# Optimization experiments

Measured on AMD Instinct MI355X. Metric: run time of the kernel, lower is better.

Reference implementation:

```python
import jax, jax.numpy as jnp
import numpy as np

# Module config (matches init_kwargs)
DIM = 256
NUM_HEADS = 8
AREA = 4
B, C, H, W = 8, DIM, 64, 64
HEAD_DIM = DIM // NUM_HEADS

# Each Conv in the source is Conv2d(bias=False) + BatchNorm2d + Identity (activation=False).
# In eval mode BN is a per-channel affine, so we represent each Conv as (weight, scale, bias).

def setup_inputs() -> dict:
    key = jax.random.key(0)
    ks = jax.random.split(key, 13)
    def w(k, shape, s=0.05):
        return jax.random.normal(k, shape, jnp.float32) * s
    def bn_scale(k, n):
        return 1.0 + 0.02 * jax.random.normal(k, (n,), jnp.float32)
    x = jax.random.normal(ks[0], (B, C, H, W), jnp.float32)
    return {
        "x": x,
        "w_qk": w(ks[1], (2 * C, C)),        # 1x1 conv: [out,in]
        "s_qk": bn_scale(ks[2], 2 * C),
        "b_qk": w(ks[3], (2 * C,), 0.01),
        "w_v": w(ks[4], (C, C)),
        "s_v": bn_scale(ks[5], C),
        "b_v": w(ks[6], (C,), 0.01),
        "w_pe": w(ks[7], (C, 1, 5, 5)),       # depthwise 5x5, groups=C
        "s_pe": bn_scale(ks[8], C),
        "b_pe": w(ks[9], (C,), 0.01),
        "w_proj": w(ks[10], (C, C)),
        "s_proj": bn_scale(ks[11], C),
        "b_proj": w(ks[12], (C,), 0.01),
    }


def _affine(y, s, b):
    # per-channel BN-eval affine on NCHW
    return y * s[None, :, None, None] + b[None, :, None, None]


def _conv1x1(x, w, s, b):
    return _affine(jnp.einsum('bchw,oc->bohw', x, w), s, b)


def reference(x, w_qk, s_qk, b_qk, w_v, s_v, b_v, w_pe, s_pe, b_pe, w_proj, s_proj, b_proj):
    N = H * W
    Na = N // AREA
    Ba = B * AREA

    qk = _conv1x1(x, w_qk, s_qk, b_qk)                    # [B, 2C, H, W]
    v4 = _conv1x1(x, w_v, s_v, b_v)                       # [B, C, H, W]
    pp = _affine(
        jax.lax.conv_general_dilated(
            v4, w_pe, (1, 1), 'SAME', feature_group_count=C,
            dimension_numbers=('NCHW', 'OIHW', 'NCHW')),
        s_pe, b_pe)                                        # [B, C, H, W]

    # flatten(2).transpose(1,2) then area split along N
    qk = qk.reshape(B, 2 * C, N).transpose(0, 2, 1).reshape(Ba, Na, 2 * C)
    v = v4.reshape(B, C, N).transpose(0, 2, 1).reshape(Ba, Na, C)

    q = qk[..., :C].reshape(Ba, Na, NUM_HEADS, HEAD_DIM)
    k = qk[..., C:].reshape(Ba, Na, NUM_HEADS, HEAD_DIM)
    vh = v.reshape(Ba, Na, NUM_HEADS, HEAD_DIM)

    scale = jnp.asarray(HEAD_DIM, jnp.float32) ** -0.5
    attn = jnp.einsum('bqhd,bkhd->bhqk', q, k) * scale     # [Ba, h, Na, Na]
    attn = jax.nn.softmax(attn, axis=-1)                   # max-stable softmax over keys
    o = jnp.einsum('bhqk,bkhd->bqhd', attn, vh)            # [Ba, Na, h, d]
    o = o.reshape(Ba, Na, C).reshape(B, N, C)
    o = o.reshape(B, H, W, C).transpose(0, 3, 1, 2)        # [B, C, H, W]

    return _conv1x1(o + pp, w_proj, s_proj, b_proj)
```

## Files before the change

### kernel.cpp

```cpp
#include <hip/hip_runtime.h>
#include <math.h>


#define NN 4096
#define NA 1024

typedef unsigned short us;
typedef __attribute__((ext_vector_type(4))) unsigned short us4;
typedef __attribute__((ext_vector_type(8))) unsigned short us8;
typedef __attribute__((ext_vector_type(8))) short bf16x8;
typedef __attribute__((ext_vector_type(4))) float f32x4;

#define QS (0.17677669529663687f * 1.4426950408889634f)

__device__ __forceinline__ us f2b(float f) {
    unsigned u = __builtin_bit_cast(unsigned, f);
    u += 0x7fffu + ((u >> 16) & 1u);
    return (us)(u >> 16);
}
__device__ __forceinline__ float b2f(us h) {
    unsigned u = ((unsigned)h) << 16;
    return __builtin_bit_cast(float, u);
}
__device__ __forceinline__ unsigned pack2(float lo, float hi) {
    return (unsigned)f2b(lo) | ((unsigned)f2b(hi) << 16);
}
__device__ __forceinline__ unsigned cvtpk_bf16(float lo, float hi) {
    unsigned r;
    asm("v_cvt_pk_bf16_f32 %0, %1, %2" : "=v"(r) : "v"(lo), "v"(hi));
    return r;
}
__device__ __forceinline__ float fexp2(float x) {
    float r;
    asm("v_exp_f32 %0, %1" : "=v"(r) : "v"(x));
    return r;
}

__device__ __forceinline__ size_t wswz(int ch, int k) {
    return ((size_t)((ch >> 4) * 8 + (k >> 5))) * 512 + ((((k >> 3) & 3) * 16 + (ch & 15))) * 8 + (k & 7);
}

__global__ __launch_bounds__(256) void prep_kernel(
    const float* __restrict__ w_qk, const float* __restrict__ s_qk, const float* __restrict__ b_qk,
    const float* __restrict__ w_v,  const float* __restrict__ s_v,
    const float* __restrict__ w_proj, const float* __restrict__ s_proj,
    us* __restrict__ wqkh, us* __restrict__ wvh, us* __restrict__ wprojh,
    float* __restrict__ bqkp)
{
    int idx = blockIdx.x * 256 + threadIdx.x;
    if (idx < 131072) {
        int o = idx >> 8, k = idx & 255;
        float sc = s_qk[o] * (o < 256 ? QS : 1.0f);
        wqkh[wswz(o, k)] = f2b(w_qk[idx] * sc);
    } else if (idx < 196608) {
        int j = idx - 131072; int o = j >> 8, k = j & 255;
        wvh[wswz(o, k)] = f2b(w_v[j] * s_v[o]);
    } else {
        int j = idx - 196608; int o = j >> 8, k = j & 255;
        wprojh[wswz(o, k)] = f2b(w_proj[j] * s_proj[o]);
    }
    if (idx < 512) bqkp[idx] = b_qk[idx] * (idx < 256 ? QS : 1.0f);
}

__global__ __launch_bounds__(256) void qkv_kernel(
    const float* __restrict__ x,
    const us* __restrict__ wqkh, const float* __restrict__ bqkp,
    const us* __restrict__ wvh,  const float* __restrict__ b_v,
    us* __restrict__ qt, us* __restrict__ vbuf)
{
    const int n0 = blockIdx.x * 64;
    const int b  = blockIdx.y;
    const int tid = threadIdx.x;
    const int w = tid >> 6, lane = tid & 63, c = lane & 15, g = lane >> 4;

    __shared__ __align__(16) us Xs[64][264];

    const float* Xb = x + (size_t)b * 256 * NN;
    #pragma unroll
    for (int i = 0; i < 16; i++) {
        int t = tid + i * 256;
        int cp = t >> 5, pp = t & 31;
        const float* r0 = Xb + (size_t)(2 * cp) * NN + n0 + 2 * pp;
        float2 a0 = *(const float2*)r0;
        float2 a1 = *(const float2*)(r0 + NN);
        *(unsigned*)&Xs[2 * pp][2 * cp]     = pack2(a0.x, a1.x);
        *(unsigned*)&Xs[2 * pp + 1][2 * cp] = pack2(a0.y, a1.y);
    }
    __syncthreads();

    for (int grp = 0; grp < 3; grp++) {
        f32x4 acc[4][4] = {};
        for (int kc = 0; kc < 256; kc += 32) {
            bf16x8 Xf[4];
            #pragma unroll
            for (int j = 0; j < 4; j++)
                Xf[j] = *(const bf16x8*)&Xs[j * 16 + c][kc + g * 8];
            #pragma unroll
            for (int cgi = 0; cgi < 4; cgi++) {
                int chbase = (grp < 2 ? (grp * 4 + cgi) * 64 : cgi * 64);
                const us* Wp = (grp < 2 ? wqkh : wvh) +
                    ((size_t)(((chbase >> 4) + w) * 8 + (kc >> 5))) * 512 + lane * 8;
                bf16x8 Wf = *(const bf16x8*)Wp;
                if (grp < 2) {
                    #pragma unroll
                    for (int j = 0; j < 4; j++)
                        acc[cgi][j] = __builtin_amdgcn_mfma_f32_16x16x32_bf16(Xf[j], Wf, acc[cgi][j], 0, 0, 0);
                } else {
                    #pragma unroll
                    for (int j = 0; j < 4; j++)
                        acc[cgi][j] = __builtin_amdgcn_mfma_f32_16x16x32_bf16(Wf, Xf[j], acc[cgi][j], 0, 0, 0);
                }
            }
        }
        if (grp < 2) {
            #pragma unroll
            for (int cgi = 0; cgi < 4; cgi++) {
                int ch = (grp * 4 + cgi) * 64 + w * 16 + c;
                float bb = bqkp[ch];
                #pragma unroll
                for (int j = 0; j < 4; j++)
                    #pragma unroll
                    for (int r = 0; r < 4; r++)
                        qt[((size_t)b * 4096 + n0 + j * 16 + g * 4 + r) * 512 + ch] =
                            f2b(acc[cgi][j][r] + bb);
            }
        } else {
            #pragma unroll
            for (int cgi = 0; cgi < 4; cgi++)
                #pragma unroll
                for (int r = 0; r < 4; r++) {
                    int ch = cgi * 64 + w * 16 + g * 4 + r;
                    float bb = b_v[ch];
                    #pragma unroll
                    for (int j = 0; j < 4; j++)
                        vbuf[((size_t)b * 256 + ch) * NN + n0 + j * 16 + c] =
                            f2b(acc[cgi][j][r] + bb);
                }
        }
    }
}

__global__ __launch_bounds__(256) void pe_conv_kernel(
    const us* __restrict__ vbuf,
    const float* __restrict__ w_pe, const float* __restrict__ s_pe, const float* __restrict__ b_pe,
    us* __restrict__ opp)
{
    const int c = blockIdx.x, b = blockIdx.y;
    const int tid = threadIdx.x;
    const us* vp = vbuf + ((size_t)b * 256 + c) * NN;
    __shared__ __align__(16) float plane[4096];
    __shared__ float wloc[25];
    #pragma unroll
    for (int i = 0; i < 4; i++) {
        int idx = tid + i * 256;
        us4 v = *(const us4*)&vp[idx * 4];
        float4 f;
        f.x = b2f(v[0]); f.y = b2f(v[1]); f.z = b2f(v[2]); f.w = b2f(v[3]);
        *(float4*)&plane[idx * 4] = f;
    }
    if (tid < 25) wloc[tid] = w_pe[c * 25 + tid];
    __syncthreads();

    const float s = s_pe[c], bb = b_pe[c];
    us* op = opp + ((size_t)b * 256 + c) * NN;
    const int r0 = tid >> 3;
    const int c0 = (tid & 7) * 8;

    #pragma unroll
    for (int i = 0; i < 2; i++) {
        const int r = r0 + i * 32;
        float acc[8] = {};
        #pragma unroll
        for (int dy = -2; dy <= 2; dy++) {
            int hy = r + dy;
            if (hy < 0 || hy > 63) continue;
            const float* rp = &plane[hy * 64];
            float wnd[16];
            float4 A, B_, C_, D;
            if (c0 >= 4) A = *(const float4*)&rp[c0 - 4];
            else         A = float4{0.f, 0.f, 0.f, 0.f};
            B_ = *(const float4*)&rp[c0];
            C_ = *(const float4*)&rp[c0 + 4];
            if (c0 <= 52) D = *(const float4*)&rp[c0 + 8];
            else          D = float4{0.f, 0.f, 0.f, 0.f};
            wnd[0] = A.x;  wnd[1] = A.y;  wnd[2] = A.z;  wnd[3] = A.w;
            wnd[4] = B_.x; wnd[5] = B_.y; wnd[6] = B_.z; wnd[7] = B_.w;
            wnd[8] = C_.x; wnd[9] = C_.y; wnd[10] = C_.z; wnd[11] = C_.w;
            wnd[12] = D.x; wnd[13] = D.y; wnd[14] = D.z; wnd[15] = D.w;
            #pragma unroll
            for (int dx = -2; dx <= 2; dx++) {
                float wv = wloc[(dy + 2) * 5 + (dx + 2)];
                #pragma unroll
                for (int j = 0; j < 8; j++)
                    acc[j] = fmaf(wnd[4 + j + dx], wv, acc[j]);
            }
        }
        us8 o;
        #pragma unroll
        for (int j = 0; j < 4; j++) {
            unsigned pr = cvtpk_bf16(acc[2 * j] * s + bb, acc[2 * j + 1] * s + bb);
            o[2 * j]     = (us)(pr & 0xFFFFu);
            o[2 * j + 1] = (us)(pr >> 16);
        }
        *(us8*)&op[r * 64 + c0] = o;
    }
}

__global__ __launch_bounds__(256) void attn_kernel(
    const us* __restrict__ qt, const us* __restrict__ vbuf, us* __restrict__ opp)
{
    const int h   = blockIdx.x;
    const int qtb = blockIdx.y;
    const int ba  = blockIdx.z;
    const int b = ba >> 2, a = ba & 3;
    const int tid = threadIdx.x;
    const int w = tid >> 6, lane = tid & 63, c = lane & 15, g = lane >> 4;
    const int q0 = qtb * 128;

    __shared__ __align__(16) us Kt[2][64][40];
    __shared__ __align__(16) us Vs[2][2048];
    __shared__ __align__(16) us Ps[128][72];

    const int krow = tid >> 2, kseg = tid & 3;
    const int vrow = tid >> 3, vseg = tid & 7;
    const int vbyte = vrow * 128 + ((vseg ^ (vrow & 7)) << 4);

    const us* Kg = qt + ((size_t)b * 4096 + a * NA) * 512 + 256 + h * 32;
    const us* Vg = vbuf + ((size_t)b * 256 + h * 32) * NN + a * NA;

    const us* Qp = qt + ((size_t)b * 4096 + a * NA + q0 + w * 16 + c) * 512 + h * 32 + g * 8;
    const bf16x8 Qf0 = *(const bf16x8*)Qp;
    const bf16x8 Qf1 = *(const bf16x8*)(Qp + (size_t)64 * 512);

    {
        us8 kreg = *(const us8*)(Kg + (size_t)krow * 512 + kseg * 8);
        us8 vreg = *(const us8*)(Vg + (size_t)vrow * NN + vseg * 8);
        *(us8*)&Kt[0][krow][kseg * 8] = kreg;
        *(us8*)((char*)Vs[0] + vbyte) = vreg;
    }
    __syncthreads();

    const bf16x8 ones = {0x3F80, 0x3F80, 0x3F80, 0x3F80, 0x3F80, 0x3F80, 0x3F80, 0x3F80};
    const f32x4 z = {0.f, 0.f, 0.f, 0.f};
    const int qr0 = w * 16 + c, qr1 = 64 + w * 16 + c;

    f32x4 O0a = z, O1a = z, Osa = z;
    f32x4 O0b = z, O1b = z, Osb = z;
    int cur = 0;

    for (int kt = 0; kt < 16; kt++) {
        us8 kreg, vreg;
        if (kt < 15) {
            const int kv1 = (kt + 1) * 64;
            kreg = *(const us8*)(Kg + ((size_t)(kv1 + krow)) * 512 + kseg * 8);
            vreg = *(const us8*)(Vg + (size_t)vrow * NN + kv1 + vseg * 8);
        }

        f32x4 sA[4], sB[4];
        #pragma unroll
        for (int j = 0; j < 4; j++) {
            bf16x8 Kf = *(const bf16x8*)&Kt[cur][j * 16 + c][g * 8];
            sA[j] = __builtin_amdgcn_mfma_f32_16x16x32_bf16(Kf, Qf0, z, 0, 0, 0);
            sB[j] = __builtin_amdgcn_mfma_f32_16x16x32_bf16(Kf, Qf1, z, 0, 0, 0);
        }

        #pragma unroll
        for (int j = 0; j < 4; j++) {
            uint2 pr;
            pr.x = cvtpk_bf16(fexp2(sA[j][0]), fexp2(sA[j][1]));
            pr.y = cvtpk_bf16(fexp2(sA[j][2]), fexp2(sA[j][3]));
            *(uint2*)&Ps[qr0][j * 16 + g * 4] = pr;
        }
        asm volatile("s_waitcnt lgkmcnt(0)" ::: "memory");
        __builtin_amdgcn_sched_barrier(0);

        uint2 prb[4];
        #pragma unroll
        for (int j = 0; j < 4; j++) {
            prb[j].x = cvtpk_bf16(fexp2(sB[j][0]), fexp2(sB[j][1]));
            prb[j].y = cvtpk_bf16(fexp2(sB[j][2]), fexp2(sB[j][3]));
        }

        #pragma unroll
        for (int ks = 0; ks < 2; ks++) {
            int so = (((ks * 4 + g) ^ (c & 7)) << 4);
            bf16x8 Bv0 = *(const bf16x8*)((char*)Vs[cur] + c * 128 + so);
            bf16x8 Bv1 = *(const bf16x8*)((char*)Vs[cur] + (16 + c) * 128 + so);
            bf16x8 Ap0 = *(const bf16x8*)&Ps[qr0][ks * 32 + g * 8];
            O0a = __builtin_amdgcn_mfma_f32_16x16x32_bf16(Ap0, Bv0, O0a, 0, 0, 0);
            O1a = __builtin_amdgcn_mfma_f32_16x16x32_bf16(Ap0, Bv1, O1a, 0, 0, 0);
            Osa = __builtin_amdgcn_mfma_f32_16x16x32_bf16(Ap0, ones, Osa, 0, 0, 0);
        }

        #pragma unroll
        for (int j = 0; j < 4; j++)
            *(uint2*)&Ps[qr1][j * 16 + g * 4] = prb[j];
        asm volatile("s_waitcnt lgkmcnt(0)" ::: "memory");
        __builtin_amdgcn_sched_barrier(0);

        #pragma unroll
        for (int ks = 0; ks < 2; ks++) {
            int so = (((ks * 4 + g) ^ (c & 7)) << 4);
            bf16x8 Bv0 = *(const bf16x8*)((char*)Vs[cur] + c * 128 + so);
            bf16x8 Bv1 = *(const bf16x8*)((char*)Vs[cur] + (16 + c) * 128 + so);
            bf16x8 Ap1 = *(const bf16x8*)&Ps[qr1][ks * 32 + g * 8];
            O0b = __builtin_amdgcn_mfma_f32_16x16x32_bf16(Ap1, Bv0, O0b, 0, 0, 0);
            O1b = __builtin_amdgcn_mfma_f32_16x16x32_bf16(Ap1, Bv1, O1b, 0, 0, 0);
            Osb = __builtin_amdgcn_mfma_f32_16x16x32_bf16(Ap1, ones, Osb, 0, 0, 0);
        }

        if (kt < 15) {
            *(us8*)&Kt[cur ^ 1][krow][kseg * 8] = kreg;
            *(us8*)((char*)Vs[cur ^ 1] + vbyte) = vreg;
        }
        __syncthreads();
        cur ^= 1;
    }

    float linva[4], linvb[4];
    #pragma unroll
    for (int r = 0; r < 4; r++) { linva[r] = 1.0f / Osa[r]; linvb[r] = 1.0f / Osb[r]; }

    us* Ob = opp + ((size_t)(b * 256 + h * 32)) * NN + a * NA + q0 + w * 16 + g * 4;
    {
        us4 o = *(us4*)(Ob + (size_t)c * NN);
        #pragma unroll
        for (int r = 0; r < 4; r++) o[r] = f2b(b2f(o[r]) + O0a[r] * linva[r]);
        *(us4*)(Ob + (size_t)c * NN) = o;
        us4 o2 = *(us4*)(Ob + (size_t)(16 + c) * NN);
        #pragma unroll
        for (int r = 0; r < 4; r++) o2[r] = f2b(b2f(o2[r]) + O1a[r] * linva[r]);
        *(us4*)(Ob + (size_t)(16 + c) * NN) = o2;

        us* Ob2 = Ob + 64;
        us4 o3 = *(us4*)(Ob2 + (size_t)c * NN);
        #pragma unroll
        for (int r = 0; r < 4; r++) o3[r] = f2b(b2f(o3[r]) + O0b[r] * linvb[r]);
        *(us4*)(Ob2 + (size_t)c * NN) = o3;
        us4 o4 = *(us4*)(Ob2 + (size_t)(16 + c) * NN);
        #pragma unroll
        for (int r = 0; r < 4; r++) o4[r] = f2b(b2f(o4[r]) + O1b[r] * linvb[r]);
        *(us4*)(Ob2 + (size_t)(16 + c) * NN) = o4;
    }
}

__global__ __launch_bounds__(256) void proj_kernel(
    const us* __restrict__ opp,
    const us* __restrict__ wprojh, const float* __restrict__ b_proj,
    float* __restrict__ out)
{
    const int n0 = blockIdx.x * 64;
    const int b  = blockIdx.y;
    const int tid = threadIdx.x;
    const int w = tid >> 6, lane = tid & 63, c = lane & 15, g = lane >> 4;

    __shared__ __align__(16) us Xs[64][264];

    const us* Xb = opp + (size_t)b * 256 * NN;
    #pragma unroll
    for (int i = 0; i < 16; i++) {
        int t = tid + i * 256;
        int cp = t >> 5, pp = t & 31;
        unsigned a0 = *(const unsigned*)&Xb[(size_t)(2 * cp) * NN + n0 + 2 * pp];
        unsigned a1 = *(const unsigned*)&Xb[(size_t)(2 * cp + 1) * NN + n0 + 2 * pp];
        *(unsigned*)&Xs[2 * pp][2 * cp]     = (a0 & 0xFFFFu) | (a1 << 16);
        *(unsigned*)&Xs[2 * pp + 1][2 * cp] = (a0 >> 16) | (a1 & 0xFFFF0000u);
    }
    __syncthreads();

    f32x4 acc[4][4] = {};
    for (int kc = 0; kc < 256; kc += 32) {
        bf16x8 Xf[4];
        #pragma unroll
        for (int j = 0; j < 4; j++)
            Xf[j] = *(const bf16x8*)&Xs[j * 16 + c][kc + g * 8];
        #pragma unroll
        for (int cgi = 0; cgi < 4; cgi++) {
            const us* Wp = wprojh +
                ((size_t)((cgi * 4 + w) * 8 + (kc >> 5))) * 512 + lane * 8;
            bf16x8 Wf = *(const bf16x8*)Wp;
            #pragma unroll
            for (int j = 0; j < 4; j++)
                acc[cgi][j] = __builtin_amdgcn_mfma_f32_16x16x32_bf16(Wf, Xf[j], acc[cgi][j], 0, 0, 0);
        }
    }

    #pragma unroll
    for (int cgi = 0; cgi < 4; cgi++)
        #pragma unroll
        for (int r = 0; r < 4; r++) {
            int ch = cgi * 64 + w * 16 + g * 4 + r;
            float bb = b_proj[ch];
            #pragma unroll
            for (int j = 0; j < 4; j++)
                out[((size_t)b * 256 + ch) * NN + n0 + j * 16 + c] = acc[cgi][j][r] + bb;
        }
}

extern "C" void kernel_launch(void* const* d_in, const int* in_sizes, int n_in,
                              void* d_out, int out_size, void* d_ws, size_t ws_size,
                              hipStream_t stream) {
    const float* x      = (const float*)d_in[0];
    const float* w_qk   = (const float*)d_in[1];
    const float* s_qk   = (const float*)d_in[2];
    const float* b_qk   = (const float*)d_in[3];
    const float* w_v    = (const float*)d_in[4];
    const float* s_v    = (const float*)d_in[5];
    const float* b_v    = (const float*)d_in[6];
    const float* w_pe   = (const float*)d_in[7];
    const float* s_pe   = (const float*)d_in[8];
    const float* b_pe   = (const float*)d_in[9];
    const float* w_proj = (const float*)d_in[10];
    const float* s_proj = (const float*)d_in[11];
    const float* b_proj = (const float*)d_in[12];
    float* out = (float*)d_out;

    char* p = (char*)d_ws;
    us* qtb     = (us*)p;                  p += (size_t)8 * 4096 * 512 * 2;
    us* vbuf    = (us*)p;                  p += (size_t)8 * 256 * 4096 * 2;
    us* opp     = (us*)p;                  p += (size_t)8 * 256 * 4096 * 2;
    us* wqkh    = (us*)p;                  p += (size_t)512 * 256 * 2;
    us* wvh     = (us*)p;                  p += (size_t)256 * 256 * 2;
    us* wprojh  = (us*)p;                  p += (size_t)256 * 256 * 2;
    float* bqkp = (float*)p;

    prep_kernel<<<1024, 256, 0, stream>>>(w_qk, s_qk, b_qk, w_v, s_v,
                                          w_proj, s_proj, wqkh, wvh, wprojh, bqkp);
    qkv_kernel<<<dim3(64, 8), 256, 0, stream>>>(x, wqkh, bqkp, wvh, b_v, qtb, vbuf);
    pe_conv_kernel<<<dim3(256, 8), 256, 0, stream>>>(vbuf, w_pe, s_pe, b_pe, opp);
    attn_kernel<<<dim3(8, 8, 32), 256, 0, stream>>>(qtb, vbuf, opp);
    proj_kernel<<<dim3(64, 8), 256, 0, stream>>>(opp, wprojh, b_proj, out);
}
```

Measured before the change: 151.3 us.

## Double query tile per attention block to reuse K/V tiles across 256 queries

Each attention block now handles 256 queries instead of 128, processing two passes of 128 queries per key tile, so each K/V tile load from global memory is reused twice as much. The grid shrinks from 8x8x32 to 8x4x32 blocks. This cuts global K/V traffic and barrier overhead per query, but raises register pressure (4 Q fragments and 12 accumulators) and halves the block count, which may reduce occupancy and parallelism.

```diff
diff --git a/kernel.cpp b/kernel.cpp
--- a/kernel.cpp
+++ b/kernel.cpp
@@ -215,7 +215,7 @@
     const int b = ba >> 2, a = ba & 3;
     const int tid = threadIdx.x;
     const int w = tid >> 6, lane = tid & 63, c = lane & 15, g = lane >> 4;
-    const int q0 = qtb * 128;
+    const int q0 = qtb * 256;
 
     __shared__ __align__(16) us Kt[2][64][40];
     __shared__ __align__(16) us Vs[2][2048];
@@ -229,8 +229,9 @@
     const us* Vg = vbuf + ((size_t)b * 256 + h * 32) * NN + a * NA;
 
     const us* Qp = qt + ((size_t)b * 4096 + a * NA + q0 + w * 16 + c) * 512 + h * 32 + g * 8;
-    const bf16x8 Qf0 = *(const bf16x8*)Qp;
-    const bf16x8 Qf1 = *(const bf16x8*)(Qp + (size_t)64 * 512);
+    bf16x8 Qf[4];
+    #pragma unroll
+    for (int hv = 0; hv < 4; hv++) Qf[hv] = *(const bf16x8*)(Qp + (size_t)(hv * 64) * 512);
 
     {
         us8 kreg = *(const us8*)(Kg + (size_t)krow * 512 + kseg * 8);
@@ -244,8 +245,9 @@
     const f32x4 z = {0.f, 0.f, 0.f, 0.f};
     const int qr0 = w * 16 + c, qr1 = 64 + w * 16 + c;
 
-    f32x4 O0a = z, O1a = z, Osa = z;
-    f32x4 O0b = z, O1b = z, Osb = z;
+    f32x4 O0[4], O1[4], Os[4];
+    #pragma unroll
+    for (int hv = 0; hv < 4; hv++) { O0[hv] = z; O1[hv] = z; Os[hv] = z; }
     int cur = 0;
 
     for (int kt = 0; kt < 16; kt++) {
@@ -256,57 +258,51 @@
             vreg = *(const us8*)(Vg + (size_t)vrow * NN + kv1 + vseg * 8);
         }
 
-        f32x4 sA[4], sB[4];
-        #pragma unroll
-        for (int j = 0; j < 4; j++) {
-            bf16x8 Kf = *(const bf16x8*)&Kt[cur][j * 16 + c][g * 8];
-            sA[j] = __builtin_amdgcn_mfma_f32_16x16x32_bf16(Kf, Qf0, z, 0, 0, 0);
-            sB[j] = __builtin_amdgcn_mfma_f32_16x16x32_bf16(Kf, Qf1, z, 0, 0, 0);
-        }
-
-        #pragma unroll
-        for (int j = 0; j < 4; j++) {
-            uint2 pr;
-            pr.x = cvtpk_bf16(fexp2(sA[j][0]), fexp2(sA[j][1]));
-            pr.y = cvtpk_bf16(fexp2(sA[j][2]), fexp2(sA[j][3]));
-            *(uint2*)&Ps[qr0][j * 16 + g * 4] = pr;
-        }
-        asm volatile("s_waitcnt lgkmcnt(0)" ::: "memory");
-        __builtin_amdgcn_sched_barrier(0);
-
-        uint2 prb[4];
-        #pragma unroll
-        for (int j = 0; j < 4; j++) {
-            prb[j].x = cvtpk_bf16(fexp2(sB[j][0]), fexp2(sB[j][1]));
-            prb[j].y = cvtpk_bf16(fexp2(sB[j][2]), fexp2(sB[j][3]));
-        }
-
-        #pragma unroll
-        for (int ks = 0; ks < 2; ks++) {
-            int so = (((ks * 4 + g) ^ (c & 7)) << 4);
-            bf16x8 Bv0 = *(const bf16x8*)((char*)Vs[cur] + c * 128 + so);
-            bf16x8 Bv1 = *(const bf16x8*)((char*)Vs[cur] + (16 + c) * 128 + so);
-            bf16x8 Ap0 = *(const bf16x8*)&Ps[qr0][ks * 32 + g * 8];
-            O0a = __builtin_amdgcn_mfma_f32_16x16x32_bf16(Ap0, Bv0, O0a, 0, 0, 0);
-            O1a = __builtin_amdgcn_mfma_f32_16x16x32_bf16(Ap0, Bv1, O1a, 0, 0, 0);
-            Osa = __builtin_amdgcn_mfma_f32_16x16x32_bf16(Ap0, ones, Osa, 0, 0, 0);
-        }
-
-        #pragma unroll
-        for (int j = 0; j < 4; j++)
-            *(uint2*)&Ps[qr1][j * 16 + g * 4] = prb[j];
-        asm volatile("s_waitcnt lgkmcnt(0)" ::: "memory");
-        __builtin_amdgcn_sched_barrier(0);
-
-        #pragma unroll
-        for (int ks = 0; ks < 2; ks++) {
-            int so = (((ks * 4 + g) ^ (c & 7)) << 4);
-            bf16x8 Bv0 = *(const bf16x8*)((char*)Vs[cur] + c * 128 + so);
-            bf16x8 Bv1 = *(const bf16x8*)((char*)Vs[cur] + (16 + c) * 128 + so);
-            bf16x8 Ap1 = *(const bf16x8*)&Ps[qr1][ks * 32 + g * 8];
-            O0b = __builtin_amdgcn_mfma_f32_16x16x32_bf16(Ap1, Bv0, O0b, 0, 0, 0);
-            O1b = __builtin_amdgcn_mfma_f32_16x16x32_bf16(Ap1, Bv1, O1b, 0, 0, 0);
-            Osb = __builtin_amdgcn_mfma_f32_16x16x32_bf16(Ap1, ones, Osb, 0, 0, 0);
+        #pragma unroll
+        for (int pass = 0; pass < 2; pass++) {
+            const int h0 = pass * 2, h1 = pass * 2 + 1;
+
+            f32x4 s0[4], s1[4];
+            #pragma unroll
+            for (int j = 0; j < 4; j++) {
+                bf16x8 Kf = *(const bf16x8*)&Kt[cur][j * 16 + c][g * 8];
+                s0[j] = __builtin_amdgcn_mfma_f32_16x16x32_bf16(Kf, Qf[h0], z, 0, 0, 0);
+                s1[j] = __builtin_amdgcn_mfma_f32_16x16x32_bf16(Kf, Qf[h1], z, 0, 0, 0);
+            }
+
+            if (pass == 1) {
+                asm volatile("s_waitcnt lgkmcnt(0)" ::: "memory");
+                __builtin_amdgcn_sched_barrier(0);
+            }
+
+            #pragma unroll
+            for (int j = 0; j < 4; j++) {
+                uint2 pr;
+                pr.x = cvtpk_bf16(fexp2(s0[j][0]), fexp2(s0[j][1]));
+                pr.y = cvtpk_bf16(fexp2(s0[j][2]), fexp2(s0[j][3]));
+                *(uint2*)&Ps[qr0][j * 16 + g * 4] = pr;
+                uint2 qr_;
+                qr_.x = cvtpk_bf16(fexp2(s1[j][0]), fexp2(s1[j][1]));
+                qr_.y = cvtpk_bf16(fexp2(s1[j][2]), fexp2(s1[j][3]));
+                *(uint2*)&Ps[qr1][j * 16 + g * 4] = qr_;
+            }
+            asm volatile("s_waitcnt lgkmcnt(0)" ::: "memory");
+            __builtin_amdgcn_sched_barrier(0);
+
+            #pragma unroll
+            for (int ks = 0; ks < 2; ks++) {
+                int so = (((ks * 4 + g) ^ (c & 7)) << 4);
+                bf16x8 Bv0 = *(const bf16x8*)((char*)Vs[cur] + c * 128 + so);
+                bf16x8 Bv1 = *(const bf16x8*)((char*)Vs[cur] + (16 + c) * 128 + so);
+                bf16x8 Ap0 = *(const bf16x8*)&Ps[qr0][ks * 32 + g * 8];
+                bf16x8 Ap1 = *(const bf16x8*)&Ps[qr1][ks * 32 + g * 8];
+                O0[h0] = __builtin_amdgcn_mfma_f32_16x16x32_bf16(Ap0, Bv0, O0[h0], 0, 0, 0);
+                O1[h0] = __builtin_amdgcn_mfma_f32_16x16x32_bf16(Ap0, Bv1, O1[h0], 0, 0, 0);
+                Os[h0] = __builtin_amdgcn_mfma_f32_16x16x32_bf16(Ap0, ones, Os[h0], 0, 0, 0);
+                O0[h1] = __builtin_amdgcn_mfma_f32_16x16x32_bf16(Ap1, Bv0, O0[h1], 0, 0, 0);
+                O1[h1] = __builtin_amdgcn_mfma_f32_16x16x32_bf16(Ap1, Bv1, O1[h1], 0, 0, 0);
+                Os[h1] = __builtin_amdgcn_mfma_f32_16x16x32_bf16(Ap1, ones, Os[h1], 0, 0, 0);
+            }
         }
 
         if (kt < 15) {
@@ -317,30 +313,20 @@
         cur ^= 1;
     }
 
-    float linva[4], linvb[4];
-    #pragma unroll
-    for (int r = 0; r < 4; r++) { linva[r] = 1.0f / Osa[r]; linvb[r] = 1.0f / Osb[r]; }
-
-    us* Ob = opp + ((size_t)(b * 256 + h * 32)) * NN + a * NA + q0 + w * 16 + g * 4;
-    {
+    #pragma unroll
+    for (int hv = 0; hv < 4; hv++) {
+        float linv[4];
+        #pragma unroll
+        for (int r = 0; r < 4; r++) linv[r] = 1.0f / Os[hv][r];
+        us* Ob = opp + ((size_t)(b * 256 + h * 32)) * NN + a * NA + q0 + hv * 64 + w * 16 + g * 4;
         us4 o = *(us4*)(Ob + (size_t)c * NN);
         #pragma unroll
-        for (int r = 0; r < 4; r++) o[r] = f2b(b2f(o[r]) + O0a[r] * linva[r]);
+        for (int r = 0; r < 4; r++) o[r] = f2b(b2f(o[r]) + O0[hv][r] * linv[r]);
         *(us4*)(Ob + (size_t)c * NN) = o;
         us4 o2 = *(us4*)(Ob + (size_t)(16 + c) * NN);
         #pragma unroll
-        for (int r = 0; r < 4; r++) o2[r] = f2b(b2f(o2[r]) + O1a[r] * linva[r]);
+        for (int r = 0; r < 4; r++) o2[r] = f2b(b2f(o2[r]) + O1[hv][r] * linv[r]);
         *(us4*)(Ob + (size_t)(16 + c) * NN) = o2;
-
-        us* Ob2 = Ob + 64;
-        us4 o3 = *(us4*)(Ob2 + (size_t)c * NN);
-        #pragma unroll
-        for (int r = 0; r < 4; r++) o3[r] = f2b(b2f(o3[r]) + O0b[r] * linvb[r]);
-        *(us4*)(Ob2 + (size_t)c * NN) = o3;
-        us4 o4 = *(us4*)(Ob2 + (size_t)(16 + c) * NN);
-        #pragma unroll
-        for (int r = 0; r < 4; r++) o4[r] = f2b(b2f(o4[r]) + O1b[r] * linvb[r]);
-        *(us4*)(Ob2 + (size_t)(16 + c) * NN) = o4;
     }
 }
 
@@ -428,6 +414,6 @@
                                           w_proj, s_proj, wqkh, wvh, wprojh, bqkp);
     qkv_kernel<<<dim3(64, 8), 256, 0, stream>>>(x, wqkh, bqkp, wvh, b_v, qtb, vbuf);
     pe_conv_kernel<<<dim3(256, 8), 256, 0, stream>>>(vbuf, w_pe, s_pe, b_pe, opp);
-    attn_kernel<<<dim3(8, 8, 32), 256, 0, stream>>>(qtb, vbuf, opp);
+    attn_kernel<<<dim3(8, 4, 32), 256, 0, stream>>>(qtb, vbuf, opp);
     proj_kernel<<<dim3(64, 8), 256, 0, stream>>>(opp, wprojh, b_proj, out);
 }
```

Result: slower. 156.9 us (+3.7%).
